# Kernel optimization log

Hardware: AMD Instinct MI355X
Metric: run time of the kernel (lower is better)

## Reference

```python
import jax, jax.numpy as jnp
import numpy as np

NF4_LEVELS = jnp.array([-1.0, -0.6962, -0.5251, -0.3949, -0.2844, -0.1848, -0.0911, 0.0,
                        0.0796, 0.1609, 0.2461, 0.3379, 0.4407, 0.5626, 0.723, 1.0], dtype=jnp.float32)
OUT_FEATURES = 4096
IN_FEATURES = 4096
BLOCK_SIZE = 1024
NUM_BLOCKS = OUT_FEATURES * IN_FEATURES // BLOCK_SIZE  # 16384

def setup_inputs() -> dict:
    key = jax.random.key(0)
    k1, k2, k3 = jax.random.split(key, 3)
    x = jax.random.normal(k1, (4, 2048, IN_FEATURES), dtype=jnp.float32)
    quant_indices = jax.random.randint(k2, (NUM_BLOCKS, BLOCK_SIZE), 0, 16, dtype=jnp.int32)
    scales = jax.random.uniform(k3, (NUM_BLOCKS,), dtype=jnp.float32)
    return {"x": x, "quant_indices": quant_indices, "scales": scales}

def reference(x, quant_indices, scales):
    # Block-wise NF4 dequantization: levels lookup * per-block absmax scale
    deq = NF4_LEVELS[quant_indices] * scales[:, None]          # [num_blocks, block_size]
    W = deq.reshape(OUT_FEATURES, IN_FEATURES)                 # [out, in]
    # F.linear(x, W): y = x @ W.T
    return jnp.einsum('bsi,oi->bso', x, W)
```

## Files before the change

kernel.cpp:

```cpp
#include <hip/hip_runtime.h>

typedef unsigned short u16;
typedef __attribute__((ext_vector_type(4))) float  f32x4;
typedef __attribute__((ext_vector_type(4))) int    i32x4;
typedef __attribute__((ext_vector_type(4))) unsigned u32x4;
typedef __attribute__((ext_vector_type(8))) short  shortx8;

__device__ __constant__ float NF4C[16] = {
    -1.0f, -0.6962f, -0.5251f, -0.3949f, -0.2844f, -0.1848f, -0.0911f, 0.0f,
     0.0796f, 0.1609f, 0.2461f, 0.3379f, 0.4407f, 0.5626f, 0.723f, 1.0f};

__device__ __forceinline__ unsigned f2bf(float f) {
    unsigned u = __float_as_uint(f);
    return (u + 0x7FFFu + ((u >> 16) & 1u)) >> 16;
}

__device__ __forceinline__ void ld_lds16(const u16* g, u16* l) {
    __builtin_amdgcn_global_load_lds(
        (const __attribute__((address_space(1))) void*)g,
        (__attribute__((address_space(3))) void*)l,
        16, 0, 0);
}


__global__ __launch_bounds__(256) void cvt_x(const float* __restrict__ x,
                                             u16* __restrict__ xb) {
    const size_t i = ((size_t)blockIdx.x * 256 + threadIdx.x) * 8;
    f32x4 f0 = __builtin_nontemporal_load((const f32x4*)(x + i));
    f32x4 f1 = __builtin_nontemporal_load((const f32x4*)(x + i + 4));
    u32x4 o;
    o[0] = f2bf(f0[0]) | (f2bf(f0[1]) << 16);
    o[1] = f2bf(f0[2]) | (f2bf(f0[3]) << 16);
    o[2] = f2bf(f1[0]) | (f2bf(f1[1]) << 16);
    o[3] = f2bf(f1[2]) | (f2bf(f1[3]) << 16);
    *(u32x4*)(xb + i) = o;
}

__global__ __launch_bounds__(256) void deq_w(const int* __restrict__ qi,
                                             const float* __restrict__ sc,
                                             u16* __restrict__ wb) {
    const size_t i = ((size_t)blockIdx.x * 256 + threadIdx.x) * 8;
    const float s = sc[i >> 10];
    i32x4 q0 = __builtin_nontemporal_load((const i32x4*)(qi + i));
    i32x4 q1 = __builtin_nontemporal_load((const i32x4*)(qi + i + 4));
    u32x4 o;
    o[0] = f2bf(NF4C[q0[0]] * s) | (f2bf(NF4C[q0[1]] * s) << 16);
    o[1] = f2bf(NF4C[q0[2]] * s) | (f2bf(NF4C[q0[3]] * s) << 16);
    o[2] = f2bf(NF4C[q1[0]] * s) | (f2bf(NF4C[q1[1]] * s) << 16);
    o[3] = f2bf(NF4C[q1[2]] * s) | (f2bf(NF4C[q1[3]] * s) << 16);
    *(u32x4*)(wb + i) = o;
}


#define BM 256
#define BN 128
#define BK 32

__global__ __launch_bounds__(256, 2) void gemm_bt(const u16* __restrict__ A,
                                                  const u16* __restrict__ B,
                                                  float* __restrict__ C) {
    constexpr int K = 4096, N = 4096;
    __shared__ __align__(16) u16 As[BM * BK];
    __shared__ __align__(16) u16 Bs[BN * BK];

    const int t    = threadIdx.x;
    const int wave = t >> 6;
    const int lane = t & 63;
    const int quad = lane >> 4;
    const int r16  = lane & 15;

    const int id  = blockIdx.x;
    const int xcd = id & 7;
    const int loc = id >> 3;
    const int bm  = (xcd * 4 + (loc >> 5)) * BM;
    const int bn  = (loc & 31) * BN;

    const int srow = t >> 2;
    const int csw  = (((t & 3) ^ ((t >> 3) & 3))) * 8;
    const u16* ga = A + (size_t)(bm + srow) * K + csw;
    const u16* gb = B + (size_t)(bn + srow) * K + csw;
    u16* la = &As[wave * 512];
    u16* lb = &Bs[wave * 512];

    const int wm = (wave >> 1) * 128;
    const int wn = (wave & 1) * 64;

    const int xsw = (quad ^ ((r16 >> 1) & 3)) * 8;

    f32x4 acc[8][4];
#pragma unroll
    for (int i = 0; i < 8; i++)
#pragma unroll
        for (int j = 0; j < 4; j++) acc[i][j] = (f32x4)0.0f;

    for (int kt = 0; kt < K / BK; ++kt) {
        ld_lds16(ga,             la);
        ld_lds16(ga +  64 * K,   la + 2048);
        ld_lds16(ga + 128 * K,   la + 4096);
        ld_lds16(ga + 192 * K,   la + 6144);
        ld_lds16(gb,             lb);
        ld_lds16(gb +  64 * K,   lb + 2048);
        ga += BK;
        gb += BK;
        __syncthreads();

        shortx8 af[8], bf[4];
#pragma unroll
        for (int i = 0; i < 8; i++)
            af[i] = *(const shortx8*)&As[(wm + i * 16 + r16) * BK + xsw];
#pragma unroll
        for (int j = 0; j < 4; j++)
            bf[j] = *(const shortx8*)&Bs[(wn + j * 16 + r16) * BK + xsw];

#pragma unroll
        for (int i = 0; i < 8; i++)
#pragma unroll
            for (int j = 0; j < 4; j++)
                acc[i][j] = __builtin_amdgcn_mfma_f32_16x16x32_bf16(
                    af[i], bf[j], acc[i][j], 0, 0, 0);
        __syncthreads();
    }

#pragma unroll
    for (int i = 0; i < 8; i++) {
        const int row0 = bm + wm + i * 16 + quad * 4;
#pragma unroll
        for (int j = 0; j < 4; j++) {
            const int col = bn + wn + j * 16 + r16;
            float* cp = &C[(size_t)row0 * N + col];
#pragma unroll
            for (int v = 0; v < 4; ++v)
                cp[(size_t)v * N] = acc[i][j][v];
        }
    }
}


__global__ __launch_bounds__(256) void fallback_gemm(const float* __restrict__ x,
                                                     const int* __restrict__ qi,
                                                     const float* __restrict__ sc,
                                                     float* __restrict__ y) {
    __shared__ float xs[16][16];
    __shared__ float wsm[16][17];
    const int tx = threadIdx.x, ty = threadIdx.y;
    const int m = blockIdx.y * 16 + ty;
    const int nrow = blockIdx.x * 16 + ty;
    float acc = 0.f;
    for (int k0 = 0; k0 < 4096; k0 += 16) {
        xs[ty][tx] = x[(size_t)m * 4096 + k0 + tx];
        const size_t fi = (size_t)nrow * 4096 + k0 + tx;
        wsm[ty][tx] = NF4C[qi[fi]] * sc[fi >> 10];
        __syncthreads();
#pragma unroll
        for (int kk = 0; kk < 16; kk++) acc += xs[ty][kk] * wsm[tx][kk];
        __syncthreads();
    }
    y[(size_t)m * 4096 + blockIdx.x * 16 + tx] = acc;
}


extern "C" void kernel_launch(void* const* d_in, const int* in_sizes, int n_in,
                              void* d_out, int out_size, void* d_ws, size_t ws_size,
                              hipStream_t stream) {
    const float* x  = (const float*)d_in[0];
    const int*   qi = (const int*)d_in[1];
    const float* sc = (const float*)d_in[2];
    float* y = (float*)d_out;

    const int M = 8192, N = 4096, K = 4096;
    const size_t xb_bytes = (size_t)M * K * 2;
    const size_t wb_bytes = (size_t)N * K * 2;

    if (ws_size >= xb_bytes + wb_bytes) {
        u16* xb = (u16*)d_ws;
        u16* wb = (u16*)((char*)d_ws + xb_bytes);
        cvt_x<<<(M * K) / (256 * 8), 256, 0, stream>>>(x, xb);
        deq_w<<<(N * K) / (256 * 8), 256, 0, stream>>>(qi, sc, wb);
        gemm_bt<<<(M / BM) * (N / BN), 256, 0, stream>>>(xb, wb, y);
    } else {
        dim3 block(16, 16);
        dim3 grid(N / 16, M / 16);
        fallback_gemm<<<grid, block, 0, stream>>>(x, qi, sc, y);
    }
}
```

Before: 518.4 us.

## Use 256x256 tiles with 8 waves and a 4-stage LDS pipeline

```diff
diff --git a/kernel.cpp b/kernel.cpp
--- a/kernel.cpp
+++ b/kernel.cpp
@@ -53,15 +53,73 @@
 
 
 #define BM 256
-#define BN 128
+#define BN 256
 #define BK 32
 
-__global__ __launch_bounds__(256, 2) void gemm_bt(const u16* __restrict__ A,
+template<bool STAGE, int VMC>
+__device__ __forceinline__ void ktile(const u16* Ar, const u16* Br,
+                                      const u16* gsa, const u16* gsb,
+                                      u16* lda, u16* ldb,
+                                      int wm128, int wn64, int r16, int xsw,
+                                      f32x4 (&acc)[8][4]) {
+    constexpr int K = 4096;
+    shortx8 af[4], bf[4], ag[4];
+
+#pragma unroll
+    for (int i = 0; i < 4; i++)
+        af[i] = *(const shortx8*)&Ar[(wm128 + i * 16 + r16) * BK + xsw];
+#pragma unroll
+    for (int j = 0; j < 4; j++)
+        bf[j] = *(const shortx8*)&Br[(wn64 + j * 16 + r16) * BK + xsw];
+    if constexpr (STAGE) {
+        ld_lds16(gsa,           lda);
+        ld_lds16(gsa + 128 * K, lda + 4096);
+    }
+    __builtin_amdgcn_s_barrier();
+    asm volatile("s_waitcnt lgkmcnt(0)" ::: "memory");
+    __builtin_amdgcn_sched_barrier(0);
+    __builtin_amdgcn_s_setprio(1);
+#pragma unroll
+    for (int i = 0; i < 4; i++)
+#pragma unroll
+        for (int j = 0; j < 4; j++)
+            acc[i][j] = __builtin_amdgcn_mfma_f32_16x16x32_bf16(
+                af[i], bf[j], acc[i][j], 0, 0, 0);
+    __builtin_amdgcn_s_setprio(0);
+    __builtin_amdgcn_s_barrier();
+
+#pragma unroll
+    for (int i = 0; i < 4; i++)
+        ag[i] = *(const shortx8*)&Ar[(wm128 + 64 + i * 16 + r16) * BK + xsw];
+    if constexpr (STAGE) {
+        ld_lds16(gsb,           ldb);
+        ld_lds16(gsb + 128 * K, ldb + 4096);
+    }
+    __builtin_amdgcn_s_barrier();
+    asm volatile("s_waitcnt lgkmcnt(0)" ::: "memory");
+    __builtin_amdgcn_sched_barrier(0);
+    __builtin_amdgcn_s_setprio(1);
+#pragma unroll
+    for (int i = 0; i < 4; i++)
+#pragma unroll
+        for (int j = 0; j < 4; j++)
+            acc[4 + i][j] = __builtin_amdgcn_mfma_f32_16x16x32_bf16(
+                ag[i], bf[j], acc[4 + i][j], 0, 0, 0);
+    __builtin_amdgcn_s_setprio(0);
+    if constexpr (VMC == 4) {
+        asm volatile("s_waitcnt vmcnt(4)" ::: "memory");
+    } else if constexpr (VMC == 0) {
+        asm volatile("s_waitcnt vmcnt(0)" ::: "memory");
+    }
+    __builtin_amdgcn_s_barrier();
+}
+
+__global__ __launch_bounds__(512, 2) void gemm_bt(const u16* __restrict__ A,
                                                   const u16* __restrict__ B,
                                                   float* __restrict__ C) {
     constexpr int K = 4096, N = 4096;
-    __shared__ __align__(16) u16 As[BM * BK];
-    __shared__ __align__(16) u16 Bs[BN * BK];
+    __shared__ __align__(16) u16 As[4][BM * BK];
+    __shared__ __align__(16) u16 Bs[4][BN * BK];
 
     const int t    = threadIdx.x;
     const int wave = t >> 6;
@@ -72,20 +130,18 @@
     const int id  = blockIdx.x;
     const int xcd = id & 7;
     const int loc = id >> 3;
-    const int bm  = (xcd * 4 + (loc >> 5)) * BM;
-    const int bn  = (loc & 31) * BN;
+    const int bm  = (xcd * 4 + (loc >> 4)) * BM;
+    const int bn  = (loc & 15) * BN;
 
     const int srow = t >> 2;
     const int csw  = (((t & 3) ^ ((t >> 3) & 3))) * 8;
-    const u16* ga = A + (size_t)(bm + srow) * K + csw;
-    const u16* gb = B + (size_t)(bn + srow) * K + csw;
-    u16* la = &As[wave * 512];
-    u16* lb = &Bs[wave * 512];
-
-    const int wm = (wave >> 1) * 128;
-    const int wn = (wave & 1) * 64;
-
-    const int xsw = (quad ^ ((r16 >> 1) & 3)) * 8;
+    const u16* gA0 = A + (size_t)(bm + srow) * K + csw;
+    const u16* gB0 = B + (size_t)(bn + srow) * K + csw;
+
+    const int wm128 = (wave >> 2) * 128;
+    const int wn64  = (wave & 3) * 64;
+    const int xsw   = (quad ^ ((r16 >> 1) & 3)) * 8;
+    const int lbase = wave * 512;
 
     f32x4 acc[8][4];
 #pragma unroll
@@ -93,40 +149,40 @@
 #pragma unroll
         for (int j = 0; j < 4; j++) acc[i][j] = (f32x4)0.0f;
 
-    for (int kt = 0; kt < K / BK; ++kt) {
-        ld_lds16(ga,             la);
-        ld_lds16(ga +  64 * K,   la + 2048);
-        ld_lds16(ga + 128 * K,   la + 4096);
-        ld_lds16(ga + 192 * K,   la + 6144);
-        ld_lds16(gb,             lb);
-        ld_lds16(gb +  64 * K,   lb + 2048);
-        ga += BK;
-        gb += BK;
-        __syncthreads();
-
-        shortx8 af[8], bf[4];
-#pragma unroll
-        for (int i = 0; i < 8; i++)
-            af[i] = *(const shortx8*)&As[(wm + i * 16 + r16) * BK + xsw];
-#pragma unroll
-        for (int j = 0; j < 4; j++)
-            bf[j] = *(const shortx8*)&Bs[(wn + j * 16 + r16) * BK + xsw];
-
-#pragma unroll
-        for (int i = 0; i < 8; i++)
-#pragma unroll
-            for (int j = 0; j < 4; j++)
-                acc[i][j] = __builtin_amdgcn_mfma_f32_16x16x32_bf16(
-                    af[i], bf[j], acc[i][j], 0, 0, 0);
-        __syncthreads();
-    }
+    ld_lds16(gA0,                &As[0][lbase]);
+    ld_lds16(gA0 + 128 * K,      &As[0][lbase + 4096]);
+    ld_lds16(gB0,                &Bs[0][lbase]);
+    ld_lds16(gB0 + 128 * K,      &Bs[0][lbase + 4096]);
+    ld_lds16(gA0 + BK,           &As[1][lbase]);
+    ld_lds16(gA0 + BK + 128 * K, &As[1][lbase + 4096]);
+    ld_lds16(gB0 + BK,           &Bs[1][lbase]);
+    ld_lds16(gB0 + BK + 128 * K, &Bs[1][lbase + 4096]);
+    asm volatile("s_waitcnt vmcnt(4)" ::: "memory");
+    __builtin_amdgcn_s_barrier();
+
+    const u16* gsa = gA0 + 2 * BK;
+    const u16* gsb = gB0 + 2 * BK;
+#pragma unroll 1
+    for (int kt = 0; kt < 126; ++kt) {
+        const int rd = kt & 3;
+        const int st = (kt + 2) & 3;
+        ktile<true, 4>(&As[rd][0], &Bs[rd][0], gsa, gsb,
+                       &As[st][lbase], &Bs[st][lbase],
+                       wm128, wn64, r16, xsw, acc);
+        gsa += BK;
+        gsb += BK;
+    }
+    ktile<false, 0>(&As[126 & 3][0], &Bs[126 & 3][0], nullptr, nullptr,
+                    nullptr, nullptr, wm128, wn64, r16, xsw, acc);
+    ktile<false, -1>(&As[127 & 3][0], &Bs[127 & 3][0], nullptr, nullptr,
+                     nullptr, nullptr, wm128, wn64, r16, xsw, acc);
 
 #pragma unroll
     for (int i = 0; i < 8; i++) {
-        const int row0 = bm + wm + i * 16 + quad * 4;
+        const int row0 = bm + wm128 + i * 16 + quad * 4;
 #pragma unroll
         for (int j = 0; j < 4; j++) {
-            const int col = bn + wn + j * 16 + r16;
+            const int col = bn + wn64 + j * 16 + r16;
             float* cp = &C[(size_t)row0 * N + col];
 #pragma unroll
             for (int v = 0; v < 4; ++v)
@@ -176,7 +232,7 @@
         u16* wb = (u16*)((char*)d_ws + xb_bytes);
         cvt_x<<<(M * K) / (256 * 8), 256, 0, stream>>>(x, xb);
         deq_w<<<(N * K) / (256 * 8), 256, 0, stream>>>(qi, sc, wb);
-        gemm_bt<<<(M / BM) * (N / BN), 256, 0, stream>>>(xb, wb, y);
+        gemm_bt<<<(M / BM) * (N / BN), 512, 0, stream>>>(xb, wb, y);
     } else {
         dim3 block(16, 16);
         dim3 grid(N / 16, M / 16);
```

New measurement: 534.4 us. +3.1%, slower.

## Triple-buffer LDS tiles in GEMM with async prefetch and single barrier per k-step

Applied to the files above, without the earlier changes.

```diff
diff --git a/kernel.cpp b/kernel.cpp
--- a/kernel.cpp
+++ b/kernel.cpp
@@ -55,13 +55,55 @@
 #define BM 256
 #define BN 128
 #define BK 32
+#define SLOT_A (BM * BK)
+#define SLOT_B (BN * BK)
+
+template<int RD, int ST, int VMC>
+__device__ __forceinline__ void ktile(const u16* gsa, const u16* gsb,
+                                      u16* Asb, u16* Bsb, int lao,
+                                      int wm, int wn, int r16, int xsw,
+                                      f32x4 (&acc)[8][4]) {
+    constexpr int K = 4096;
+    if constexpr (ST >= 0) {
+        u16* la = Asb + ST * SLOT_A + lao;
+        u16* lb = Bsb + ST * SLOT_B + lao;
+        ld_lds16(gsa,           la);
+        ld_lds16(gsa +  64 * K, la + 2048);
+        ld_lds16(gsa + 128 * K, la + 4096);
+        ld_lds16(gsa + 192 * K, la + 6144);
+        ld_lds16(gsb,           lb);
+        ld_lds16(gsb +  64 * K, lb + 2048);
+    }
+    const u16* Ar = Asb + RD * SLOT_A;
+    const u16* Br = Bsb + RD * SLOT_B;
+    shortx8 af[8], bf[4];
+#pragma unroll
+    for (int i = 0; i < 8; i++)
+        af[i] = *(const shortx8*)&Ar[(wm + i * 16 + r16) * BK + xsw];
+#pragma unroll
+    for (int j = 0; j < 4; j++)
+        bf[j] = *(const shortx8*)&Br[(wn + j * 16 + r16) * BK + xsw];
+#pragma unroll
+    for (int i = 0; i < 8; i++)
+#pragma unroll
+        for (int j = 0; j < 4; j++)
+            acc[i][j] = __builtin_amdgcn_mfma_f32_16x16x32_bf16(
+                af[i], bf[j], acc[i][j], 0, 0, 0);
+    if constexpr (VMC == 6) {
+        asm volatile("s_waitcnt vmcnt(6)" ::: "memory");
+        asm volatile("s_barrier" ::: "memory");
+    } else if constexpr (VMC == 0) {
+        asm volatile("s_waitcnt vmcnt(0)" ::: "memory");
+        asm volatile("s_barrier" ::: "memory");
+    }
+}
 
 __global__ __launch_bounds__(256, 2) void gemm_bt(const u16* __restrict__ A,
                                                   const u16* __restrict__ B,
                                                   float* __restrict__ C) {
     constexpr int K = 4096, N = 4096;
-    __shared__ __align__(16) u16 As[BM * BK];
-    __shared__ __align__(16) u16 Bs[BN * BK];
+    __shared__ __align__(16) u16 As[3 * SLOT_A];
+    __shared__ __align__(16) u16 Bs[3 * SLOT_B];
 
     const int t    = threadIdx.x;
     const int wave = t >> 6;
@@ -77,14 +119,12 @@
 
     const int srow = t >> 2;
     const int csw  = (((t & 3) ^ ((t >> 3) & 3))) * 8;
-    const u16* ga = A + (size_t)(bm + srow) * K + csw;
-    const u16* gb = B + (size_t)(bn + srow) * K + csw;
-    u16* la = &As[wave * 512];
-    u16* lb = &Bs[wave * 512];
+    const u16* gA0 = A + (size_t)(bm + srow) * K + csw;
+    const u16* gB0 = B + (size_t)(bn + srow) * K + csw;
+    const int lao  = wave * 512;
 
     const int wm = (wave >> 1) * 128;
     const int wn = (wave & 1) * 64;
-
     const int xsw = (quad ^ ((r16 >> 1) & 3)) * 8;
 
     f32x4 acc[8][4];
@@ -93,33 +133,40 @@
 #pragma unroll
         for (int j = 0; j < 4; j++) acc[i][j] = (f32x4)0.0f;
 
-    for (int kt = 0; kt < K / BK; ++kt) {
-        ld_lds16(ga,             la);
-        ld_lds16(ga +  64 * K,   la + 2048);
-        ld_lds16(ga + 128 * K,   la + 4096);
-        ld_lds16(ga + 192 * K,   la + 6144);
-        ld_lds16(gb,             lb);
-        ld_lds16(gb +  64 * K,   lb + 2048);
-        ga += BK;
-        gb += BK;
-        __syncthreads();
-
-        shortx8 af[8], bf[4];
-#pragma unroll
-        for (int i = 0; i < 8; i++)
-            af[i] = *(const shortx8*)&As[(wm + i * 16 + r16) * BK + xsw];
-#pragma unroll
-        for (int j = 0; j < 4; j++)
-            bf[j] = *(const shortx8*)&Bs[(wn + j * 16 + r16) * BK + xsw];
-
-#pragma unroll
-        for (int i = 0; i < 8; i++)
-#pragma unroll
-            for (int j = 0; j < 4; j++)
-                acc[i][j] = __builtin_amdgcn_mfma_f32_16x16x32_bf16(
-                    af[i], bf[j], acc[i][j], 0, 0, 0);
-        __syncthreads();
-    }
+    {
+        u16* la = &As[lao];
+        u16* lb = &Bs[lao];
+        ld_lds16(gA0,           la);
+        ld_lds16(gA0 +  64 * K, la + 2048);
+        ld_lds16(gA0 + 128 * K, la + 4096);
+        ld_lds16(gA0 + 192 * K, la + 6144);
+        ld_lds16(gB0,           lb);
+        ld_lds16(gB0 +  64 * K, lb + 2048);
+        la = &As[SLOT_A + lao];
+        lb = &Bs[SLOT_B + lao];
+        ld_lds16(gA0 + BK,           la);
+        ld_lds16(gA0 + BK +  64 * K, la + 2048);
+        ld_lds16(gA0 + BK + 128 * K, la + 4096);
+        ld_lds16(gA0 + BK + 192 * K, la + 6144);
+        ld_lds16(gB0 + BK,           lb);
+        ld_lds16(gB0 + BK +  64 * K, lb + 2048);
+    }
+    asm volatile("s_waitcnt vmcnt(6)" ::: "memory");
+    asm volatile("s_barrier" ::: "memory");
+
+    const u16* gsa = gA0 + 2 * BK;
+    const u16* gsb = gB0 + 2 * BK;
+#pragma unroll 1
+    for (int kt = 0; kt < 126; kt += 3) {
+        ktile<0, 2, 6>(gsa, gsb, As, Bs, lao, wm, wn, r16, xsw, acc);
+        gsa += BK; gsb += BK;
+        ktile<1, 0, 6>(gsa, gsb, As, Bs, lao, wm, wn, r16, xsw, acc);
+        gsa += BK; gsb += BK;
+        ktile<2, 1, 6>(gsa, gsb, As, Bs, lao, wm, wn, r16, xsw, acc);
+        gsa += BK; gsb += BK;
+    }
+    ktile<0, -1, 0>(nullptr, nullptr, As, Bs, lao, wm, wn, r16, xsw, acc);
+    ktile<1, -1, -1>(nullptr, nullptr, As, Bs, lao, wm, wn, r16, xsw, acc);
 
 #pragma unroll
     for (int i = 0; i < 8; i++) {
```

New measurement: 513.6 us. About the same (-0.9%).

## Double-buffer LDS with interleaved async loads in a 256x256x64 GEMM tile

Applied to the files above, without the earlier changes.

```diff
diff --git a/kernel.cpp b/kernel.cpp
--- a/kernel.cpp
+++ b/kernel.cpp
@@ -53,15 +53,110 @@
 
 
 #define BM 256
-#define BN 128
-#define BK 32
-
-__global__ __launch_bounds__(256, 2) void gemm_bt(const u16* __restrict__ A,
+#define BN 256
+#define BK 64
+
+template<int MODE>
+__device__ __forceinline__ void kgroup(
+    const u16* __restrict__ Ar, const u16* __restrict__ Br,
+    u16* dA1, u16* dB1,
+    u16* dBc,
+    const u16* gA1, const u16* gB1,
+    int wm, int wn, int r16, int c0, int c1,
+    f32x4 (&acc)[8][4])
+{
+    constexpr size_t K = 4096;
+    shortx8 a[4], b[4];
+
+#pragma unroll
+    for (int j = 0; j < 4; j++)
+        b[j] = *(const shortx8*)&Br[(wn + j * 16 + r16) * 64 + c0 * 8];
+#pragma unroll
+    for (int i = 0; i < 4; i++)
+        a[i] = *(const shortx8*)&Ar[(wm + i * 16 + r16) * 64 + c0 * 8];
+    if constexpr (MODE <= 1) {
+        ld_lds16(gB1 + 128 * K, dB1 + 128 * 64);
+        ld_lds16(gB1 + 192 * K, dB1 + 192 * 64);
+    }
+    asm volatile("s_barrier" ::: "memory");
+    asm volatile("s_waitcnt lgkmcnt(0)" ::: "memory");
+    __builtin_amdgcn_s_setprio(1);
+#pragma unroll
+    for (int i = 0; i < 4; i++)
+#pragma unroll
+        for (int j = 0; j < 4; j++)
+            acc[i][j] = __builtin_amdgcn_mfma_f32_16x16x32_bf16(a[i], b[j], acc[i][j], 0, 0, 0);
+    __builtin_amdgcn_s_setprio(0);
+    if constexpr (MODE <= 1) asm volatile("s_waitcnt vmcnt(4)" ::: "memory");
+    asm volatile("s_barrier" ::: "memory");
+
+#pragma unroll
+    for (int i = 0; i < 4; i++)
+        a[i] = *(const shortx8*)&Ar[(wm + 64 + i * 16 + r16) * 64 + c0 * 8];
+    if constexpr (MODE <= 1) {
+        ld_lds16(gA1,           dA1);
+        ld_lds16(gA1 + 128 * K, dA1 + 128 * 64);
+    }
+    asm volatile("s_barrier" ::: "memory");
+    asm volatile("s_waitcnt lgkmcnt(0)" ::: "memory");
+    __builtin_amdgcn_s_setprio(1);
+#pragma unroll
+    for (int i = 0; i < 4; i++)
+#pragma unroll
+        for (int j = 0; j < 4; j++)
+            acc[4 + i][j] = __builtin_amdgcn_mfma_f32_16x16x32_bf16(a[i], b[j], acc[4 + i][j], 0, 0, 0);
+    __builtin_amdgcn_s_setprio(0);
+    asm volatile("s_barrier" ::: "memory");
+
+#pragma unroll
+    for (int j = 0; j < 4; j++)
+        b[j] = *(const shortx8*)&Br[(wn + j * 16 + r16) * 64 + c1 * 8];
+#pragma unroll
+    for (int i = 0; i < 4; i++)
+        a[i] = *(const shortx8*)&Ar[(wm + i * 16 + r16) * 64 + c1 * 8];
+    if constexpr (MODE <= 1) {
+        ld_lds16(gA1 +  64 * K, dA1 +  64 * 64);
+        ld_lds16(gA1 + 192 * K, dA1 + 192 * 64);
+    }
+    asm volatile("s_barrier" ::: "memory");
+    asm volatile("s_waitcnt lgkmcnt(0)" ::: "memory");
+    __builtin_amdgcn_s_setprio(1);
+#pragma unroll
+    for (int i = 0; i < 4; i++)
+#pragma unroll
+        for (int j = 0; j < 4; j++)
+            acc[i][j] = __builtin_amdgcn_mfma_f32_16x16x32_bf16(a[i], b[j], acc[i][j], 0, 0, 0);
+    __builtin_amdgcn_s_setprio(0);
+    asm volatile("s_barrier" ::: "memory");
+
+#pragma unroll
+    for (int i = 0; i < 4; i++)
+        a[i] = *(const shortx8*)&Ar[(wm + 64 + i * 16 + r16) * 64 + c1 * 8];
+    if constexpr (MODE == 0) {
+        ld_lds16(gB1 + 64,           dBc);
+        ld_lds16(gB1 + 64 + 64 * K,  dBc + 64 * 64);
+    }
+    asm volatile("s_barrier" ::: "memory");
+    asm volatile("s_waitcnt lgkmcnt(0)" ::: "memory");
+    __builtin_amdgcn_s_setprio(1);
+#pragma unroll
+    for (int i = 0; i < 4; i++)
+#pragma unroll
+        for (int j = 0; j < 4; j++)
+            acc[4 + i][j] = __builtin_amdgcn_mfma_f32_16x16x32_bf16(a[i], b[j], acc[4 + i][j], 0, 0, 0);
+    __builtin_amdgcn_s_setprio(0);
+    if constexpr (MODE == 0)      asm volatile("s_waitcnt vmcnt(4)" ::: "memory");
+    else if constexpr (MODE == 1) asm volatile("s_waitcnt vmcnt(0)" ::: "memory");
+    asm volatile("s_barrier" ::: "memory");
+}
+
+__global__ __launch_bounds__(512, 2) void gemm_bt(const u16* __restrict__ A,
                                                   const u16* __restrict__ B,
                                                   float* __restrict__ C) {
-    constexpr int K = 4096, N = 4096;
-    __shared__ __align__(16) u16 As[BM * BK];
-    __shared__ __align__(16) u16 Bs[BN * BK];
+    constexpr size_t K = 4096;
+    constexpr int N = 4096;
+    __shared__ __align__(16) u16 As[2][BM * BK];
+    __shared__ __align__(16) u16 Bs[2][BN * BK];
 
     const int t    = threadIdx.x;
     const int wave = t >> 6;
@@ -72,20 +167,22 @@
     const int id  = blockIdx.x;
     const int xcd = id & 7;
     const int loc = id >> 3;
-    const int bm  = (xcd * 4 + (loc >> 5)) * BM;
-    const int bn  = (loc & 31) * BN;
-
-    const int srow = t >> 2;
-    const int csw  = (((t & 3) ^ ((t >> 3) & 3))) * 8;
-    const u16* ga = A + (size_t)(bm + srow) * K + csw;
-    const u16* gb = B + (size_t)(bn + srow) * K + csw;
-    u16* la = &As[wave * 512];
-    u16* lb = &Bs[wave * 512];
-
-    const int wm = (wave >> 1) * 128;
-    const int wn = (wave & 1) * 64;
-
-    const int xsw = (quad ^ ((r16 >> 1) & 3)) * 8;
+    const int bm  = (xcd * 4 + (loc >> 4)) * BM;
+    const int bn  = (loc & 15) * BN;
+
+    const int lrow = (wave << 3) + (lane >> 3);
+    const int lch  = (lane & 7) ^ (lane >> 3);
+    const u16* sA = A + (size_t)(bm + lrow) * K + lch * 8;
+    const u16* sB = B + (size_t)(bn + lrow) * K + lch * 8;
+
+    const int w512 = wave * 512;
+    u16* dA0 = &As[0][w512];  u16* dA1 = &As[1][w512];
+    u16* dB0 = &Bs[0][w512];  u16* dB1 = &Bs[1][w512];
+
+    const int wm = (wave >> 2) * 128;
+    const int wn = (wave & 3) * 64;
+    const int c0 = quad ^ (r16 & 7);
+    const int c1 = c0 ^ 4;
 
     f32x4 acc[8][4];
 #pragma unroll
@@ -93,33 +190,27 @@
 #pragma unroll
         for (int j = 0; j < 4; j++) acc[i][j] = (f32x4)0.0f;
 
-    for (int kt = 0; kt < K / BK; ++kt) {
-        ld_lds16(ga,             la);
-        ld_lds16(ga +  64 * K,   la + 2048);
-        ld_lds16(ga + 128 * K,   la + 4096);
-        ld_lds16(ga + 192 * K,   la + 6144);
-        ld_lds16(gb,             lb);
-        ld_lds16(gb +  64 * K,   lb + 2048);
-        ga += BK;
-        gb += BK;
-        __syncthreads();
-
-        shortx8 af[8], bf[4];
-#pragma unroll
-        for (int i = 0; i < 8; i++)
-            af[i] = *(const shortx8*)&As[(wm + i * 16 + r16) * BK + xsw];
-#pragma unroll
-        for (int j = 0; j < 4; j++)
-            bf[j] = *(const shortx8*)&Bs[(wn + j * 16 + r16) * BK + xsw];
-
-#pragma unroll
-        for (int i = 0; i < 8; i++)
-#pragma unroll
-            for (int j = 0; j < 4; j++)
-                acc[i][j] = __builtin_amdgcn_mfma_f32_16x16x32_bf16(
-                    af[i], bf[j], acc[i][j], 0, 0, 0);
-        __syncthreads();
-    }
+#pragma unroll
+    for (int r0 = 0; r0 < 256; r0 += 64) {
+        ld_lds16(sA + (size_t)r0 * K, dA0 + r0 * 64);
+        ld_lds16(sB + (size_t)r0 * K, dB0 + r0 * 64);
+    }
+    ld_lds16(sB + 64,                 dB1);
+    ld_lds16(sB + 64 + (size_t)64 * K, dB1 + 64 * 64);
+    asm volatile("s_waitcnt vmcnt(2)" ::: "memory");
+    asm volatile("s_barrier" ::: "memory");
+
+    const u16* gA1 = sA + 64;
+    const u16* gB1 = sB + 64;
+#pragma unroll 1
+    for (int u = 0; u < 62; u += 2) {
+        kgroup<0>(As[0], Bs[0], dA1, dB1, dB0, gA1, gB1, wm, wn, r16, c0, c1, acc);
+        gA1 += 64; gB1 += 64;
+        kgroup<0>(As[1], Bs[1], dA0, dB0, dB1, gA1, gB1, wm, wn, r16, c0, c1, acc);
+        gA1 += 64; gB1 += 64;
+    }
+    kgroup<1>(As[0], Bs[0], dA1, dB1, dB0, gA1, gB1, wm, wn, r16, c0, c1, acc);
+    kgroup<2>(As[1], Bs[1], dA0, dB0, dB1, gA1, gB1, wm, wn, r16, c0, c1, acc);
 
 #pragma unroll
     for (int i = 0; i < 8; i++) {
@@ -176,7 +267,7 @@
         u16* wb = (u16*)((char*)d_ws + xb_bytes);
         cvt_x<<<(M * K) / (256 * 8), 256, 0, stream>>>(x, xb);
         deq_w<<<(N * K) / (256 * 8), 256, 0, stream>>>(qi, sc, wb);
-        gemm_bt<<<(M / BM) * (N / BN), 256, 0, stream>>>(xb, wb, y);
+        gemm_bt<<<(M / BM) * (N / BN), 512, 0, stream>>>(xb, wb, y);
     } else {
         dim3 block(16, 16);
         dim3 grid(N / 16, M / 16);
```

Result: faster. 491.8 us (-5.1%).
